# Kernel tuning notes

Measured on AMD Instinct MI355X. Metric: run time of the kernel, lower is better.

The kernel has to match this reference:

```python
import jax, jax.numpy as jnp
import numpy as np
from math import sqrt

ROPE_BASE = 6000.0


def _rope_tables(seq_len, rope_dim, dtype):
    # inv_freq: [rope_dim/2]; emb = concat(freqs, freqs) along last dim -> [seq_len, rope_dim]
    inv_freq = 1.0 / (ROPE_BASE ** (jnp.arange(0, rope_dim, 2, dtype=jnp.float32) / rope_dim))
    t = jnp.arange(seq_len, dtype=jnp.float32)
    freqs = jnp.outer(t, inv_freq)
    emb = jnp.concatenate([freqs, freqs], axis=-1)
    return jnp.cos(emb).astype(dtype), jnp.sin(emb).astype(dtype)


def _rotate_half(x):
    x1, x2 = jnp.split(x, 2, axis=-1)
    return jnp.concatenate([-x2, x1], axis=-1)


def setup_inputs() -> dict:
    key = jax.random.key(0)
    k1, k2, k3 = jax.random.split(key, 3)
    B, S, D = 2, 2048, 1024
    H, DK = 16, 64
    x = jax.random.normal(k1, (B, S, D), dtype=jnp.float32)
    W_qkv = jax.random.normal(k2, (3, H, DK, D), dtype=jnp.float32) * 0.02
    W_o = jax.random.normal(k3, (D, H * DK), dtype=jnp.float32) * 0.02
    return {"x": x, "W_qkv": W_qkv, "W_o": W_o}


def reference(x, W_qkv, W_o):
    B, S, D = x.shape
    _, H, DK, _ = W_qkv.shape
    rope_dim = DK // 2  # RotaryEmbeddings(dim=d_k // 2)

    # fused QKV projection: [B, 3, H, S, DK]
    qkv = jnp.einsum('bsm,qhdm->bqhsd', x, W_qkv)

    # inline RoPE on Q and K, first rope_dim channels only
    cos, sin = _rope_tables(S, rope_dim, x.dtype)  # [S, rope_dim]
    qk = qkv[:, :2, :, :, :rope_dim]
    qk_rot = qk * cos + _rotate_half(qk) * sin
    qkv = qkv.at[:, :2, :, :, :rope_dim].set(qk_rot)

    Q, K, V = qkv[:, 0], qkv[:, 1], qkv[:, 2]  # [B, H, S, DK]

    scores = jnp.einsum('bhqd,bhkd->bhqk', Q, K)
    causal = jnp.triu(jnp.ones((S, S), dtype=bool), k=1)
    scores = jnp.where(causal, -jnp.inf, scores) / sqrt(DK)
    attn = jax.nn.softmax(scores, axis=-1)
    out = jnp.einsum('bhqk,bhkd->bhqd', attn, V)

    # concat heads: [B, S, H*DK], then output projection (Linear weight [D, H*DK])
    out = out.transpose(0, 2, 1, 3).reshape(B, S, H * DK)
    return jnp.einsum('bsh,dh->bsd', out, W_o)
```

## Files before the change

### kernel.cpp

```cpp
#include <hip/hip_runtime.h>
#include <math.h>


static constexpr int Bb  = 2;
static constexpr int Ss  = 2048;
static constexpr int Hh  = 16;
static constexpr int DKk = 64;

static constexpr size_t QSZ = (size_t)Bb * Hh * Ss * DKk;

static constexpr size_t WOB_E  = 0;
static constexpr size_t XB_E   = 1048576;
static constexpr size_t WQKV_E = 5242880;
static constexpr size_t QB_E   = 9437184;
static constexpr size_t OB_E   = QB_E + 3*QSZ;
static constexpr size_t OP_BYTE = 2097152;
static constexpr size_t LP_BYTE = 52428800;

typedef __attribute__((ext_vector_type(8))) short short8;
typedef __attribute__((ext_vector_type(4))) float f32x4;

__device__ __forceinline__ unsigned short f2bf(float f) {
    unsigned int u = __float_as_uint(f);
    u += 0x7fffu + ((u >> 16) & 1u);
    return (unsigned short)(u >> 16);
}

__device__ __forceinline__ unsigned int cvtpk_bf16(float lo, float hi) {
    unsigned int r;
    asm("v_cvt_pk_bf16_f32 %0, %1, %2" : "=v"(r) : "v"(lo), "v"(hi));
    return r;
}

__device__ __forceinline__ float fexp2(float x) {
    float r;
    asm("v_exp_f32 %0, %1" : "=v"(r) : "v"(x));
    return r;
}

__device__ __forceinline__ float fsin_rev(float r) {
    float o;
    asm("v_sin_f32 %0, %1" : "=v"(o) : "v"(r));
    return o;
}
__device__ __forceinline__ float fcos_rev(float r) {
    float o;
    asm("v_cos_f32 %0, %1" : "=v"(o) : "v"(r));
    return o;
}

__device__ __forceinline__ void gl16(const unsigned short* g, unsigned short* l) {
    __builtin_amdgcn_global_load_lds(
        (const __attribute__((address_space(1))) void*)g,
        (__attribute__((address_space(3))) void*)l, 16, 0, 0);
}

__global__ __launch_bounds__(256)
void convert_bf16(const float* __restrict__ x, const float* __restrict__ wqkv,
                  const float* __restrict__ wo, unsigned short* __restrict__ dst,
                  float* __restrict__ Lp)
{
    if (blockIdx.x >= 8192) {
        const size_t j4 = ((size_t)(blockIdx.x - 8192) * 256 + threadIdx.x) * 4;
        *(float4*)(Lp + j4) = float4{0.f, 0.f, 0.f, 0.f};
        return;
    }
    const size_t i4 = ((size_t)blockIdx.x * 256 + threadIdx.x) * 4;
    const float* src;
    if (i4 < 1048576)      src = wo   + i4;
    else if (i4 < 5242880) src = x    + (i4 - 1048576);
    else                   src = wqkv + (i4 - 5242880);
    const float4 v = *(const float4*)src;
    ushort4 p = { f2bf(v.x), f2bf(v.y), f2bf(v.z), f2bf(v.w) };
    *(ushort4*)(dst + i4) = p;
}

template<int MODE, int BN>
__global__ __launch_bounds__(256)
void gemm_mfma(const unsigned short* __restrict__ A,
               const unsigned short* __restrict__ Bm,
               float* __restrict__ C, unsigned short* __restrict__ QKV, int N)
{
    constexpr int K   = 1024;
    constexpr int NF  = BN / 32;
    constexpr int ASZ = 128 * 32;
    constexpr int BSZ = BN * 32;
    __shared__ unsigned short ShPool[2 * ASZ + 2 * BSZ];
    unsigned short* As0 = ShPool;
    unsigned short* As1 = ShPool + ASZ;
    unsigned short* Bs0 = ShPool + 2 * ASZ;
    unsigned short* Bs1 = ShPool + 2 * ASZ + BSZ;

    const int t    = threadIdx.x;
    const int lane = t & 63;
    const int w    = t >> 6;
    const int l15  = lane & 15;
    const int quad = lane >> 4;
    const int wr   = w >> 1;
    const int wc   = w & 1;
    const int n0   = blockIdx.x * BN;
    const int m0   = blockIdx.y * 128;

    const unsigned short* Ag = A  + (size_t)(m0 + (t >> 2)) * K + (t & 3) * 8;
    const unsigned short* Bg = Bm + (size_t)(n0 + (t >> 2)) * K + (t & 3) * 8;

    f32x4 acc[4][NF];
    #pragma unroll
    for (int i = 0; i < 4; i++)
        #pragma unroll
        for (int j = 0; j < NF; j++) acc[i][j] = f32x4{0.f, 0.f, 0.f, 0.f};

    auto stage = [&](int k0, unsigned short* Asb, unsigned short* Bsb) {
        gl16(Ag + k0,        Asb + t*8);
        gl16(Ag + 64*K + k0, Asb + 2048 + t*8);
        gl16(Bg + k0,        Bsb + t*8);
        if (BN == 128) gl16(Bg + 64*K + k0, Bsb + 2048 + t*8);
    };
    auto comp = [&](const unsigned short* Asb, const unsigned short* Bsb) {
        short8 af[4], bfv[NF];
        #pragma unroll
        for (int mf = 0; mf < 4; mf++)
            af[mf] = *(const short8*)&Asb[(wr*64 + mf*16 + l15) * 32 + quad*8];
        #pragma unroll
        for (int nf = 0; nf < NF; nf++)
            bfv[nf] = *(const short8*)&Bsb[(wc*(BN/2) + nf*16 + l15) * 32 + quad*8];
        #pragma unroll
        for (int mf = 0; mf < 4; mf++)
            #pragma unroll
            for (int nf = 0; nf < NF; nf++)
                acc[mf][nf] = __builtin_amdgcn_mfma_f32_16x16x32_bf16(
                    af[mf], bfv[nf], acc[mf][nf], 0, 0, 0);
    };

    stage(0, As0, Bs0);
    for (int k0 = 0; k0 < K; k0 += 64) {
        __syncthreads();
        stage(k0 + 32, As1, Bs1);
        comp(As0, Bs0);
        __syncthreads();
        if (k0 + 64 < K) stage(k0 + 64, As0, Bs0);
        comp(As1, Bs1);
    }

    if (MODE == 0) {
        #pragma unroll
        for (int mf = 0; mf < 4; mf++)
            #pragma unroll
            for (int r = 0; r < 4; r++) {
                float* crow = C + (size_t)(m0 + wr*64 + mf*16 + quad*4 + r) * N
                            + n0 + wc*(BN/2);
                #pragma unroll
                for (int nf = 0; nf < NF; nf++)
                    crow[nf*16 + l15] = acc[mf][nf][r];
            }
    } else {
        __syncthreads();
        const int col0 = n0 + wc*64;
        const int q    = col0 >> 10;
        const int h    = (col0 >> 6) & 15;
        const int row0 = m0 + wr*64;
        const int b    = row0 >> 11;
        const int s0   = row0 & 2047;
        if (q == 2) {
            unsigned short* chunk = ShPool + w * 2048;
            unsigned short* vb = QKV + 2*QSZ
                               + (size_t)(b*Hh + h) * DKk * Ss + s0;
            #pragma unroll
            for (int pass = 0; pass < 2; pass++) {
                #pragma unroll
                for (int mf = 0; mf < 4; mf++)
                    #pragma unroll
                    for (int nfp = 0; nfp < 2; nfp++) {
                        const int nf = pass*2 + nfp;
                        const int dl = nfp*16 + l15;
                        const int sby = (mf*16 + quad*4) * 2;
                        ushort4 pv = { f2bf(acc[mf][nf][0]), f2bf(acc[mf][nf][1]),
                                       f2bf(acc[mf][nf][2]), f2bf(acc[mf][nf][3]) };
                        *(ushort4*)((char*)chunk
                            + dl*128 + (sby ^ ((dl & 7) << 4))) = pv;
                    }
                #pragma unroll
                for (int dblk = 0; dblk < 8; dblk++) {
                    const int dl = dblk*4 + quad;
                    const int sl = l15*4;
                    const ushort4 pv = *(const ushort4*)((char*)chunk
                        + dl*128 + ((sl*2) ^ ((dl & 7) << 4)));
                    *(ushort4*)(vb + (size_t)(pass*32 + dl) * Ss + sl) = pv;
                }
            }
        } else {
            const float qsc = (q == 0) ? 0.125f * 1.44269504088896f : 1.0f;
            const float rev_freq = (float)(exp(-(double)(2 * l15) / 32.0
                                   * log(6000.0)) / 6.283185307179586);
            unsigned short* base = QKV + (size_t)q * QSZ
                                 + ((size_t)(b*Hh + h) * Ss) * DKk;
            #pragma unroll
            for (int mf = 0; mf < 4; mf++)
                #pragma unroll
                for (int r = 0; r < 4; r++) {
                    const int s = s0 + mf*16 + quad*4 + r;
                    float rev = (float)s * rev_freq;
                    rev -= floorf(rev);
                    const float sn = fsin_rev(rev);
                    const float cs = fcos_rev(rev);
                    const float v0 = acc[mf][0][r] * qsc;
                    const float v1 = acc[mf][1][r] * qsc;
                    unsigned short* rowp = base + (size_t)s * DKk;
                    rowp[l15]      = f2bf(v0 * cs - v1 * sn);
                    rowp[16 + l15] = f2bf(v1 * cs + v0 * sn);
                    rowp[32 + l15] = f2bf(acc[mf][2][r] * qsc);
                    rowp[48 + l15] = f2bf(acc[mf][3][r] * qsc);
                }
        }
    }
}

__global__ __launch_bounds__(256)
void flash_mfma(const unsigned short* __restrict__ Qa,
                const unsigned short* __restrict__ Ka,
                const unsigned short* __restrict__ Va,
                float* __restrict__ Op, float* __restrict__ Lp)
{
    __shared__ unsigned short Ks0[64*64];
    __shared__ unsigned short Ks1[64*64];
    __shared__ unsigned short Vs0[64*64];
    __shared__ unsigned short Vs1[64*64];

    const int t    = threadIdx.x;
    const int lane = t & 63;
    const int w    = t >> 6;
    const int l15  = lane & 15;
    const int quad = lane >> 4;

    const int bid   = blockIdx.x;
    const int xcd   = bid & 7;
    const int slot  = bid >> 3;
    const int start = xcd*1088 + (slot < 64 ? 9*slot : 576 + 8*(slot - 64));
    const int n     = (slot < 64) ? 9 : 8;

    int bh  = start / 272;
    int rem = start - bh*272;
    int QT  = 0;
    while ((QT+1)*(QT+2) <= rem) QT++;
    int kt  = rem - QT*(QT+1);

    const int c0 = t,       r0 = c0 >> 3, g0 = ((c0 & 7) ^ (r0 & 7)) * 8;
    const int c1 = t + 256, r1 = c1 >> 3, g1 = ((c1 & 7) ^ (r1 & 7)) * 8;

    auto stage = [&](int sbh, int skt, unsigned short* Ksb, unsigned short* Vsb) {
        const unsigned short* Kg = Ka + (size_t)sbh * Ss * DKk + (size_t)skt*64*DKk;
        const unsigned short* Vg = Va + (size_t)sbh * DKk * Ss + skt*64;
        gl16(Kg + (size_t)r0*DKk + g0, Ksb + t*8);
        gl16(Kg + (size_t)r1*DKk + g1, Ksb + (t+256)*8);
        gl16(Vg + (size_t)r0*Ss  + g0, Vsb + t*8);
        gl16(Vg + (size_t)r1*Ss  + g1, Vsb + (t+256)*8);
    };

    short8 qf[2][2];
    f32x4 o[2][4];
    float lacc[2];
    auto zero_acc = [&]() {
        #pragma unroll
        for (int mfq = 0; mfq < 2; mfq++) {
            lacc[mfq] = 0.f;
            #pragma unroll
            for (int i = 0; i < 4; i++) o[mfq][i] = f32x4{0.f,0.f,0.f,0.f};
        }
    };
    auto loadQ = [&](int qbh, int qQT) {
        #pragma unroll
        for (int mfq = 0; mfq < 2; mfq++) {
            const unsigned short* qrow = Qa + (size_t)qbh * Ss * DKk
                + (size_t)(qQT*128 + w*32 + mfq*16 + l15) * DKk;
            qf[mfq][0] = *(const short8*)(qrow + quad*8);
            qf[mfq][1] = *(const short8*)(qrow + 32 + quad*8);
        }
    };
    auto flush = [&](int obh, int oQT) {
        const int b = obh >> 4, h = obh & 15;
        const int q0 = oQT*128 + w*32;
        #pragma unroll
        for (int mfq = 0; mfq < 2; mfq++) {
            float ls = lacc[mfq];
            ls += __shfl_xor(ls, 16);
            ls += __shfl_xor(ls, 32);
            if (quad == 0)
                atomicAdd(&Lp[(size_t)obh*Ss + q0 + mfq*16 + l15], ls);
            #pragma unroll
            for (int r = 0; r < 4; r++) {
                const int row = q0 + mfq*16 + quad*4 + r;
                float* orow = Op + ((size_t)b*Ss + row) * 1024 + h*64;
                #pragma unroll
                for (int dt = 0; dt < 4; dt++)
                    atomicAdd(&orow[dt*16 + l15], o[mfq][dt][r]);
            }
        }
    };
    auto compute = [&](const unsigned short* Ksb, const unsigned short* Vsb,
                       int cQT, int ckt) {
        f32x4 sc[4][2];
        #pragma unroll
        for (int nt = 0; nt < 4; nt++)
            #pragma unroll
            for (int mfq = 0; mfq < 2; mfq++) sc[nt][mfq] = f32x4{0.f,0.f,0.f,0.f};
        #pragma unroll
        for (int nt = 0; nt < 4; nt++)
            #pragma unroll
            for (int kc = 0; kc < 2; kc++) {
                const short8 kf = *(const short8*)&Ksb[(nt*16 + l15)*64
                                   + (((kc*4 + quad) ^ (l15 & 7)) * 8)];
                sc[nt][0] = __builtin_amdgcn_mfma_f32_16x16x32_bf16(kf, qf[0][kc], sc[nt][0], 0,0,0);
                sc[nt][1] = __builtin_amdgcn_mfma_f32_16x16x32_bf16(kf, qf[1][kc], sc[nt][1], 0,0,0);
            }

        if (ckt >= 2*cQT) {
            const int kb = ckt*64 + quad*4;
            const int qb = cQT*128 + w*32 + l15;
            #pragma unroll
            for (int nt = 0; nt < 4; nt++)
                #pragma unroll
                for (int mfq = 0; mfq < 2; mfq++)
                    #pragma unroll
                    for (int r = 0; r < 4; r++)
                        if (kb + nt*16 + r > qb + mfq*16)
                            sc[nt][mfq][r] = -INFINITY;
        }

        #pragma unroll
        for (int nt = 0; nt < 4; nt++)
            #pragma unroll
            for (int mfq = 0; mfq < 2; mfq++)
                #pragma unroll
                for (int r = 0; r < 4; r++)
                    sc[nt][mfq][r] = fexp2(sc[nt][mfq][r]);
        #pragma unroll
        for (int mfq = 0; mfq < 2; mfq++)
            #pragma unroll
            for (int nt = 0; nt < 4; nt++)
                lacc[mfq] += (sc[nt][mfq][0] + sc[nt][mfq][1])
                           + (sc[nt][mfq][2] + sc[nt][mfq][3]);

        short8 pfrag[2][2];
        #pragma unroll
        for (int mfq = 0; mfq < 2; mfq++)
            #pragma unroll
            for (int kc = 0; kc < 2; kc++) {
                unsigned int pk[4];
                #pragma unroll
                for (int v = 0; v < 4; v++) {
                    const int nt = 2*kc + (v >> 1);
                    const int rr = 2*(v & 1);
                    pk[v] = cvtpk_bf16(sc[nt][mfq][rr], sc[nt][mfq][rr+1]);
                }
                pfrag[mfq][kc] = *(short8*)&pk[0];
            }

        #pragma unroll
        for (int dt = 0; dt < 4; dt++) {
            const int row = dt*16 + l15;
            const int rx  = row & 7;
            const int wi  = 4*(quad & 1);
            #pragma unroll
            for (int kc = 0; kc < 2; kc++) {
                const ushort4 lo = *(const ushort4*)&Vsb[row*64
                                    + (((4*kc + (quad>>1)) ^ rx) * 8) + wi];
                const ushort4 hi = *(const ushort4*)&Vsb[row*64
                                    + (((4*kc + 2 + (quad>>1)) ^ rx) * 8) + wi];
                short8 vf;
                vf[0]=lo.x; vf[1]=lo.y; vf[2]=lo.z; vf[3]=lo.w;
                vf[4]=hi.x; vf[5]=hi.y; vf[6]=hi.z; vf[7]=hi.w;
                o[0][dt] = __builtin_amdgcn_mfma_f32_16x16x32_bf16(
                    pfrag[0][kc], vf, o[0][dt], 0,0,0);
                o[1][dt] = __builtin_amdgcn_mfma_f32_16x16x32_bf16(
                    pfrag[1][kc], vf, o[1][dt], 0,0,0);
            }
        }
    };

    int cbh = bh, cQT = QT, ckt = kt;
    int pbh = bh, pQT = QT, pkt = kt;
    auto advance = [&]() {
        pkt++;
        if (pkt == 2*pQT + 2) { pkt = 0; pQT++; if (pQT == 16) { pQT = 0; pbh++; } }
    };

    stage(pbh, pkt, Ks0, Vs0);
    advance();
    int own_bh = cbh, own_QT = cQT;
    loadQ(own_bh, own_QT);
    zero_acc();

    int i = 0;
    while (true) {
        __syncthreads();
        const bool h1 = (i + 1 < n);
        if (h1) stage(pbh, pkt, Ks1, Vs1);
        if (cbh != own_bh || cQT != own_QT) {
            flush(own_bh, own_QT); zero_acc();
            own_bh = cbh; own_QT = cQT; loadQ(own_bh, own_QT);
        }
        compute(Ks0, Vs0, cQT, ckt);
        if (!h1) break;
        cbh = pbh; cQT = pQT; ckt = pkt; advance();
        i++;
        __syncthreads();
        const bool h2 = (i + 1 < n);
        if (h2) stage(pbh, pkt, Ks0, Vs0);
        if (cbh != own_bh || cQT != own_QT) {
            flush(own_bh, own_QT); zero_acc();
            own_bh = cbh; own_QT = cQT; loadQ(own_bh, own_QT);
        }
        compute(Ks1, Vs1, cQT, ckt);
        if (!h2) break;
        cbh = pbh; cQT = pQT; ckt = pkt; advance();
        i++;
    }
    flush(own_bh, own_QT);
}

__global__ __launch_bounds__(256)
void reduce_o(const float* __restrict__ Op, const float* __restrict__ Lp,
              unsigned short* __restrict__ Ob)
{
    const size_t i4 = ((size_t)blockIdx.x * 256 + threadIdx.x) * 4;
    const int row = (int)(i4 >> 10);
    const int col = (int)(i4 & 1023);
    const int h   = col >> 6;
    const int b   = row >> 11;
    const int s   = row & 2047;
    const float inv = 1.0f / Lp[(size_t)((b << 4) + h) * Ss + s];
    const float4 v = *(const float4*)(Op + i4);
    ushort4 p = { f2bf(v.x*inv), f2bf(v.y*inv), f2bf(v.z*inv), f2bf(v.w*inv) };
    *(ushort4*)(Ob + i4) = p;
}

extern "C" void kernel_launch(void* const* d_in, const int* in_sizes, int n_in,
                              void* d_out, int out_size, void* d_ws, size_t ws_size,
                              hipStream_t stream)
{
    const float* x    = (const float*)d_in[0];
    const float* Wqkv = (const float*)d_in[1];
    const float* Wo   = (const float*)d_in[2];
    float* out = (float*)d_out;
    unsigned short* wsu = (unsigned short*)d_ws;
    float* Op = (float*)((char*)d_ws + OP_BYTE);
    float* Lp = (float*)((char*)d_ws + LP_BYTE);

    const dim3 blk(256);
    convert_bf16<<<dim3(8256), blk, 0, stream>>>(x, Wqkv, Wo, wsu, Lp);
    gemm_mfma<1,128><<<dim3(24, 32), blk, 0, stream>>>(wsu + XB_E, wsu + WQKV_E,
                                                       nullptr, wsu + QB_E, 3072);
    hipMemsetAsync((char*)d_ws + OP_BYTE, 0, 16777216, stream);
    flash_mfma<<<dim3(1024), blk, 0, stream>>>(wsu + QB_E, wsu + QB_E + QSZ,
                                               wsu + QB_E + 2*QSZ, Op, Lp);
    reduce_o<<<dim3(4096), blk, 0, stream>>>(Op, Lp, wsu + OB_E);
    gemm_mfma<0,64><<<dim3(16, 32), blk, 0, stream>>>(wsu + OB_E, wsu + WOB_E,
                                                      out, nullptr, 1024);
}
```

Baseline: 203.7 us.

## Pair causal query tiles per block and normalize output in flash kernel

Replaces the split-KV stream-K flash schedule, which used float atomics into a partial output buffer plus a separate reduce kernel, with one block per (head, query-tile pair). Each block pairs tile i with tile 15-i so every block does 34 KV steps. With each query tile owned by a single block, the kernel divides by the row sum and writes bf16 output directly. This removes the memset, the atomics, the Lp zeroing and the reduce_o kernel. Grid size drops from 1024 to 256 blocks, which lowers parallelism and lengthens per-block serial work.

```diff
diff --git a/kernel.cpp b/kernel.cpp
--- a/kernel.cpp
+++ b/kernel.cpp
@@ -14,8 +14,6 @@
 static constexpr size_t WQKV_E = 5242880;
 static constexpr size_t QB_E   = 9437184;
 static constexpr size_t OB_E   = QB_E + 3*QSZ;
-static constexpr size_t OP_BYTE = 2097152;
-static constexpr size_t LP_BYTE = 52428800;
 
 typedef __attribute__((ext_vector_type(8))) short short8;
 typedef __attribute__((ext_vector_type(4))) float f32x4;
@@ -57,14 +55,8 @@
 
 __global__ __launch_bounds__(256)
 void convert_bf16(const float* __restrict__ x, const float* __restrict__ wqkv,
-                  const float* __restrict__ wo, unsigned short* __restrict__ dst,
-                  float* __restrict__ Lp)
+                  const float* __restrict__ wo, unsigned short* __restrict__ dst)
 {
-    if (blockIdx.x >= 8192) {
-        const size_t j4 = ((size_t)(blockIdx.x - 8192) * 256 + threadIdx.x) * 4;
-        *(float4*)(Lp + j4) = float4{0.f, 0.f, 0.f, 0.f};
-        return;
-    }
     const size_t i4 = ((size_t)blockIdx.x * 256 + threadIdx.x) * 4;
     const float* src;
     if (i4 < 1048576)      src = wo   + i4;
@@ -219,7 +211,7 @@
 void flash_mfma(const unsigned short* __restrict__ Qa,
                 const unsigned short* __restrict__ Ka,
                 const unsigned short* __restrict__ Va,
-                float* __restrict__ Op, float* __restrict__ Lp)
+                unsigned short* __restrict__ Ob)
 {
     __shared__ unsigned short Ks0[64*64];
     __shared__ unsigned short Ks1[64*64];
@@ -232,24 +224,21 @@
     const int l15  = lane & 15;
     const int quad = lane >> 4;
 
-    const int bid   = blockIdx.x;
-    const int xcd   = bid & 7;
-    const int slot  = bid >> 3;
-    const int start = xcd*1088 + (slot < 64 ? 9*slot : 576 + 8*(slot - 64));
-    const int n     = (slot < 64) ? 9 : 8;
-
-    int bh  = start / 272;
-    int rem = start - bh*272;
-    int QT  = 0;
-    while ((QT+1)*(QT+2) <= rem) QT++;
-    int kt  = rem - QT*(QT+1);
+    const int bid  = blockIdx.x;
+    const int xcd  = bid & 7;
+    const int slot = bid >> 3;
+    const int bh   = xcd*4 + (slot >> 3);
+    const int pr   = slot & 7;
+    const int QTa  = pr;
+    const int QTb  = 15 - pr;
+    const int n    = 34;
 
     const int c0 = t,       r0 = c0 >> 3, g0 = ((c0 & 7) ^ (r0 & 7)) * 8;
     const int c1 = t + 256, r1 = c1 >> 3, g1 = ((c1 & 7) ^ (r1 & 7)) * 8;
 
-    auto stage = [&](int sbh, int skt, unsigned short* Ksb, unsigned short* Vsb) {
-        const unsigned short* Kg = Ka + (size_t)sbh * Ss * DKk + (size_t)skt*64*DKk;
-        const unsigned short* Vg = Va + (size_t)sbh * DKk * Ss + skt*64;
+    auto stage = [&](int skt, unsigned short* Ksb, unsigned short* Vsb) {
+        const unsigned short* Kg = Ka + (size_t)bh * Ss * DKk + (size_t)skt*64*DKk;
+        const unsigned short* Vg = Va + (size_t)bh * DKk * Ss + skt*64;
         gl16(Kg + (size_t)r0*DKk + g0, Ksb + t*8);
         gl16(Kg + (size_t)r1*DKk + g1, Ksb + (t+256)*8);
         gl16(Vg + (size_t)r0*Ss  + g0, Vsb + t*8);
@@ -267,32 +256,32 @@
             for (int i = 0; i < 4; i++) o[mfq][i] = f32x4{0.f,0.f,0.f,0.f};
         }
     };
-    auto loadQ = [&](int qbh, int qQT) {
+    auto loadQ = [&](int qQT) {
         #pragma unroll
         for (int mfq = 0; mfq < 2; mfq++) {
-            const unsigned short* qrow = Qa + (size_t)qbh * Ss * DKk
+            const unsigned short* qrow = Qa + (size_t)bh * Ss * DKk
                 + (size_t)(qQT*128 + w*32 + mfq*16 + l15) * DKk;
             qf[mfq][0] = *(const short8*)(qrow + quad*8);
             qf[mfq][1] = *(const short8*)(qrow + 32 + quad*8);
         }
     };
-    auto flush = [&](int obh, int oQT) {
-        const int b = obh >> 4, h = obh & 15;
+    auto flush = [&](int oQT) {
+        const int b = bh >> 4, h = bh & 15;
         const int q0 = oQT*128 + w*32;
         #pragma unroll
         for (int mfq = 0; mfq < 2; mfq++) {
             float ls = lacc[mfq];
             ls += __shfl_xor(ls, 16);
             ls += __shfl_xor(ls, 32);
-            if (quad == 0)
-                atomicAdd(&Lp[(size_t)obh*Ss + q0 + mfq*16 + l15], ls);
             #pragma unroll
             for (int r = 0; r < 4; r++) {
-                const int row = q0 + mfq*16 + quad*4 + r;
-                float* orow = Op + ((size_t)b*Ss + row) * 1024 + h*64;
+                const int x = quad*4 + r;
+                const float inv = 1.0f / __shfl(ls, (lane & 48) + x);
+                const int row = q0 + mfq*16 + x;
+                unsigned short* orow = Ob + ((size_t)b*Ss + row) * 1024 + h*64;
                 #pragma unroll
                 for (int dt = 0; dt < 4; dt++)
-                    atomicAdd(&orow[dt*16 + l15], o[mfq][dt][r]);
+                    orow[dt*16 + l15] = f2bf(o[mfq][dt][r] * inv);
             }
         }
     };
@@ -377,61 +366,45 @@
         }
     };
 
-    int cbh = bh, cQT = QT, ckt = kt;
-    int pbh = bh, pQT = QT, pkt = kt;
+    int cQT = QTa, ckt = 0;
+    int pQT = QTa, pkt = 0;
     auto advance = [&]() {
         pkt++;
-        if (pkt == 2*pQT + 2) { pkt = 0; pQT++; if (pQT == 16) { pQT = 0; pbh++; } }
-    };
-
-    stage(pbh, pkt, Ks0, Vs0);
+        if (pkt == 2*pQT + 2) { pkt = 0; pQT = QTb; }
+    };
+
+    stage(pkt, Ks0, Vs0);
     advance();
-    int own_bh = cbh, own_QT = cQT;
-    loadQ(own_bh, own_QT);
+    int own_QT = cQT;
+    loadQ(own_QT);
     zero_acc();
 
     int i = 0;
     while (true) {
         __syncthreads();
         const bool h1 = (i + 1 < n);
-        if (h1) stage(pbh, pkt, Ks1, Vs1);
-        if (cbh != own_bh || cQT != own_QT) {
-            flush(own_bh, own_QT); zero_acc();
-            own_bh = cbh; own_QT = cQT; loadQ(own_bh, own_QT);
+        if (h1) stage(pkt, Ks1, Vs1);
+        if (cQT != own_QT) {
+            flush(own_QT); zero_acc();
+            own_QT = cQT; loadQ(own_QT);
         }
         compute(Ks0, Vs0, cQT, ckt);
         if (!h1) break;
-        cbh = pbh; cQT = pQT; ckt = pkt; advance();
+        cQT = pQT; ckt = pkt; advance();
         i++;
         __syncthreads();
         const bool h2 = (i + 1 < n);
-        if (h2) stage(pbh, pkt, Ks0, Vs0);
-        if (cbh != own_bh || cQT != own_QT) {
-            flush(own_bh, own_QT); zero_acc();
-            own_bh = cbh; own_QT = cQT; loadQ(own_bh, own_QT);
+        if (h2) stage(pkt, Ks0, Vs0);
+        if (cQT != own_QT) {
+            flush(own_QT); zero_acc();
+            own_QT = cQT; loadQ(own_QT);
         }
         compute(Ks1, Vs1, cQT, ckt);
         if (!h2) break;
-        cbh = pbh; cQT = pQT; ckt = pkt; advance();
+        cQT = pQT; ckt = pkt; advance();
         i++;
     }
-    flush(own_bh, own_QT);
-}
-
-__global__ __launch_bounds__(256)
-void reduce_o(const float* __restrict__ Op, const float* __restrict__ Lp,
-              unsigned short* __restrict__ Ob)
-{
-    const size_t i4 = ((size_t)blockIdx.x * 256 + threadIdx.x) * 4;
-    const int row = (int)(i4 >> 10);
-    const int col = (int)(i4 & 1023);
-    const int h   = col >> 6;
-    const int b   = row >> 11;
-    const int s   = row & 2047;
-    const float inv = 1.0f / Lp[(size_t)((b << 4) + h) * Ss + s];
-    const float4 v = *(const float4*)(Op + i4);
-    ushort4 p = { f2bf(v.x*inv), f2bf(v.y*inv), f2bf(v.z*inv), f2bf(v.w*inv) };
-    *(ushort4*)(Ob + i4) = p;
+    flush(own_QT);
 }
 
 extern "C" void kernel_launch(void* const* d_in, const int* in_sizes, int n_in,
@@ -443,17 +416,13 @@
     const float* Wo   = (const float*)d_in[2];
     float* out = (float*)d_out;
     unsigned short* wsu = (unsigned short*)d_ws;
-    float* Op = (float*)((char*)d_ws + OP_BYTE);
-    float* Lp = (float*)((char*)d_ws + LP_BYTE);
 
     const dim3 blk(256);
-    convert_bf16<<<dim3(8256), blk, 0, stream>>>(x, Wqkv, Wo, wsu, Lp);
+    convert_bf16<<<dim3(8192), blk, 0, stream>>>(x, Wqkv, Wo, wsu);
     gemm_mfma<1,128><<<dim3(24, 32), blk, 0, stream>>>(wsu + XB_E, wsu + WQKV_E,
                                                        nullptr, wsu + QB_E, 3072);
-    hipMemsetAsync((char*)d_ws + OP_BYTE, 0, 16777216, stream);
-    flash_mfma<<<dim3(1024), blk, 0, stream>>>(wsu + QB_E, wsu + QB_E + QSZ,
-                                               wsu + QB_E + 2*QSZ, Op, Lp);
-    reduce_o<<<dim3(4096), blk, 0, stream>>>(Op, Lp, wsu + OB_E);
+    flash_mfma<<<dim3(256), blk, 0, stream>>>(wsu + QB_E, wsu + QB_E + QSZ,
+                                              wsu + QB_E + 2*QSZ, wsu + OB_E);
     gemm_mfma<0,64><<<dim3(16, 32), blk, 0, stream>>>(wsu + OB_E, wsu + WOB_E,
                                                       out, nullptr, 1024);
 }
```

After: 183.2 us. 1.11x faster.
